# Kernel optimization log

Hardware: AMD Instinct MI355X
Metric: run time of the kernel (lower is better)

Reference implementation:

```python
import math
import jax, jax.numpy as jnp
import numpy as np

B, C_IN, C_OUT, H, W = 8, 256, 256, 64, 64
STYLE_DIM, KSIZE = 512, 3
UP, DOWN = 2, 2          # AliasFreeActivation: upsample = layer_upsample*2 = 2, downsample = 2
N_TAPS = 12
MARGIN = 10


def _kaiser_lowpass(n_taps, cutoff, band_half, sr):
    # lowpass_filter() from the source (1D kaiser-windowed sinc)
    df = 2.0 * band_half / (sr / 2.0)
    atten = 2.285 * (n_taps - 1) * np.pi * df + 7.95
    if atten > 50:
        beta = 0.1102 * (atten - 8.7)
    elif atten >= 21:
        beta = 0.5842 * (atten - 21) ** 0.4 + 0.07886 * (atten - 21)
    else:
        beta = 0.0
    ind = np.arange(n_taps) - (n_taps - 1) / 2.0
    win = np.i0(beta * np.sqrt(1.0 - (2.0 * ind / (n_taps - 1)) ** 2)) / np.i0(beta)
    return (2.0 * cutoff / sr * np.sinc(2.0 * cutoff / sr * ind) * win).astype(np.float32)


def setup_inputs() -> dict:
    key = jax.random.key(0)
    ks = jax.random.split(key, 4)
    return {
        "input": jax.random.normal(ks[0], (B, C_IN, H, W), jnp.float32),
        "style": jax.random.normal(ks[1], (B, STYLE_DIM), jnp.float32),
        "conv_weight": jax.random.normal(ks[2], (C_OUT, C_IN, KSIZE, KSIZE), jnp.float32),
        "mod_w": jax.random.normal(ks[3], (C_IN, STYLE_DIM), jnp.float32),
        "mod_b": jnp.ones((C_IN,), jnp.float32),          # EqualLinear bias_init=1
        "bias": jnp.zeros((C_OUT,), jnp.float32),         # AliasFreeActivation bias
        "up_filter": jnp.asarray(_kaiser_lowpass(N_TAPS, 32.0, 32.0, 128.0)),
        "down_filter": jnp.asarray(_kaiser_lowpass(N_TAPS, 32.0, 32.0, 128.0)),
    }


def _upfirdn1d(x, kern, up, down, pad0, pad1, axis):
    # Separable upfirdn2d: zero-stuff by `up`, pad, TRUE convolution (flipped
    # kernel correlation), then stride-`down`. lax lhs_dilation gives (n-1)*up+1
    # samples vs torch's n*up, so fold the (up-1) trailing zeros into pad1.
    C, k = x.shape[1], kern.shape[0]
    kflip = kern[::-1]
    if axis == 3:  # width
        w = jnp.tile(kflip.reshape(1, 1, 1, k), (C, 1, 1, 1))
        strides, pad, dil = (1, down), ((0, 0), (pad0, pad1 + up - 1)), (1, up)
    else:  # height
        w = jnp.tile(kflip.reshape(1, 1, k, 1), (C, 1, 1, 1))
        strides, pad, dil = (down, 1), ((pad0, pad1 + up - 1), (0, 0)), (up, 1)
    return jax.lax.conv_general_dilated(
        x, w, strides, pad, lhs_dilation=dil, feature_group_count=C,
        dimension_numbers=('NCHW', 'OIHW', 'NCHW'))


def reference(input, style, conv_weight, mod_w, mod_b, bias, up_filter, down_filter):
    # --- ModulatedConv2d (padding=False, demodulate=True, eval: ema_var=1) ---
    scale = 1.0 / math.sqrt(C_IN * KSIZE * KSIZE)
    s = style @ (mod_w.T / math.sqrt(STYLE_DIM)) + mod_b            # (B, C_in)
    w = scale * conv_weight[None] * s[:, None, :, None, None]      # (B, C_out, C_in, k, k)
    demod = jax.lax.rsqrt(jnp.sum(w * w, axis=(2, 3, 4)) + 1e-8)
    w = w * demod[:, :, None, None, None]
    w = w / (1.0 + 1e-8)  # weight / (sqrt(ema_var) + eps), ema_var buffer = 1.0
    out = jax.vmap(lambda xi, wi: jax.lax.conv_general_dilated(
        xi[None], wi, (1, 1), 'VALID',
        dimension_numbers=('NCHW', 'OIHW', 'NCHW'))[0])(input, w)   # (B, C_out, 62, 62)

    # --- AliasFreeActivation ---
    out = out + bias.reshape(1, -1, 1, 1)
    p = N_TAPS - UP
    up0, up1 = (p + 1) // 2 + UP * 2 - 1, p // 2 + UP   # padding=False branch (k==3)
    uf = up_filter * UP                                  # 1D filter gain (applied per axis)
    out = _upfirdn1d(out, uf, UP, 1, up0, up1, axis=3)
    out = _upfirdn1d(out, uf, UP, 1, up0, up1, axis=2)   # (B, C_out, 128, 128)
    out = jnp.where(out >= 0, out, 0.2 * out) * math.sqrt(2.0)  # fused_leaky_relu
    p = N_TAPS - DOWN
    d0, d1 = (p + 1) // 2, p // 2
    out = _upfirdn1d(out, down_filter, 1, DOWN, d0, d1, axis=3)
    out = _upfirdn1d(out, down_filter, 1, DOWN, d0, d1, axis=2)  # (B, C_out, 64, 64)
    # margin crop: m = (MARGIN*UP - MARGIN*DOWN)//2 = 0 -> no crop
    return out
```

## Files before the change

kernel.cpp:

```cpp
#include <hip/hip_runtime.h>
#include <math.h>

#define B_   8
#define CIN  256
#define COUT 256
#define H_   64
#define W_   64
#define HO   62
#define WO   62
#define SDIM 512

#define CSTRIDE 64

typedef __attribute__((ext_vector_type(8))) short bf16x8;
typedef __attribute__((ext_vector_type(4))) float f32x4;

__device__ __forceinline__ unsigned short f2bf(float f) {
    unsigned int u = __float_as_uint(f);
    u += 0x7fffu + ((u >> 16) & 1u);
    return (unsigned short)(u >> 16);
}
__device__ __forceinline__ float bf2f(unsigned short h) {
    return __uint_as_float(((unsigned int)h) << 16);
}


__global__ void mod_kernel(const float* __restrict__ style, const float* __restrict__ mod_w,
                           const float* __restrict__ mod_b, float* __restrict__ s_out,
                           float* __restrict__ zpage) {
    if (blockIdx.x == 0) {
        zpage[threadIdx.x] = 0.f;
        zpage[threadIdx.x + 256] = 0.f;
    }
    int wid = blockIdx.x * 4 + (threadIdx.x >> 6);
    int lane = threadIdx.x & 63;
    int b = wid >> 8, ci = wid & 255;
    float acc = 0.f;
    const float* st = style + b * SDIM;
    const float* mw = mod_w + ci * SDIM;
    for (int i = 0; i < SDIM; i += 64) acc += st[i + lane] * mw[i + lane];
    for (int m = 32; m >= 1; m >>= 1) acc += __shfl_xor(acc, m, 64);
    if (lane == 0) s_out[wid] = acc * 0.04419417382415922f + mod_b[ci];
}

__global__ void wsplit_kernel(const float* __restrict__ cw, float* __restrict__ wsq,
                              unsigned short* __restrict__ wh) {
    int idx = blockIdx.x * blockDim.x + threadIdx.x;
    int co = idx >> 8, ci = idx & 255;
    const float* p = cw + (size_t)idx * 9;
    float ss = 0.f;
#pragma unroll
    for (int k = 0; k < 9; ++k) {
        float v = p[k];
        ss += v * v;
        wh[(k * COUT + co) * CIN + ci] = f2bf(v);
    }
    wsq[idx] = ss;
}

__global__ void demod_kernel(const float* __restrict__ s_in, const float* __restrict__ wsq,
                             float* __restrict__ dm) {
    int wid = blockIdx.x * 4 + (threadIdx.x >> 6);
    int lane = threadIdx.x & 63;
    int b = wid >> 8, co = wid & 255;
    float acc = 0.f;
    for (int i = 0; i < CIN; i += 64) {
        float sv = s_in[b * CIN + i + lane];
        acc += sv * sv * wsq[co * CIN + i + lane];
    }
    for (int m = 32; m >= 1; m >>= 1) acc += __shfl_xor(acc, m, 64);
    if (lane == 0) {
        const float scale = 0.020833333333333332f;
        float demod = rsqrtf(scale * scale * acc + 1e-8f);
        dm[wid] = demod * scale / (1.f + 1e-8f);
    }
}

__global__ __launch_bounds__(256) void xsplit_kernel(
        const float* __restrict__ x, const float* __restrict__ s_in,
        unsigned short* __restrict__ xh) {
    __shared__ float tile[128 * 65];
    __shared__ float s_loc[256];
    int b = blockIdx.x >> 6;
    int y = blockIdx.x & 63;
    int tid = threadIdx.x;
    s_loc[tid] = s_in[(b << 8) + tid];
    __syncthreads();
    for (int half = 0; half < 2; ++half) {
        int cb = half << 7;
        for (int f = tid; f < 2048; f += 256) {
            int ci = f >> 4, x4 = (f & 15) << 2;
            float4 v = *(const float4*)(x + ((((size_t)b << 8) + cb + ci) << 12) + (y << 6) + x4);
            float sv = s_loc[cb + ci];
            float* t = tile + ci * 65 + x4;
            t[0] = v.x * sv; t[1] = v.y * sv; t[2] = v.z * sv; t[3] = v.w * sv;
        }
        __syncthreads();
        for (int g = tid; g < 1024; g += 256) {
            int c = g & 15, xx = g >> 4;
            unsigned int hw[4];
#pragma unroll
            for (int q = 0; q < 4; ++q) {
                float v0 = tile[(c * 8 + 2 * q) * 65 + xx];
                float v1 = tile[(c * 8 + 2 * q + 1) * 65 + xx];
                hw[q] = (unsigned int)f2bf(v0) | ((unsigned int)f2bf(v1) << 16);
            }
            int o = ((((b << 6) + y) << 6) + xx) * 256 + cb + (c << 3);
            *(uint4*)(xh + o) = make_uint4(hw[0], hw[1], hw[2], hw[3]);
        }
        __syncthreads();
    }
}

__device__ __forceinline__ void stage_b(const unsigned short* wh, const int* bsrc,
                                        short* dst, int tid, int kyci) {
#pragma unroll
    for (int j = 0; j < 6; ++j)
        __builtin_amdgcn_global_load_lds(
            (const __attribute__((address_space(1))) unsigned int*)(wh + bsrc[j] + kyci),
            (__attribute__((address_space(3))) unsigned int*)(dst + ((tid + (j << 8)) << 3)),
            16, 0, 0);
}
__device__ __forceinline__ void stage_a(const unsigned short* a0, const unsigned short* a1,
                                        const unsigned short* a2, short* dst, int tid, int ci0) {
    __builtin_amdgcn_global_load_lds(
        (const __attribute__((address_space(1))) unsigned int*)(a0 + ci0),
        (__attribute__((address_space(3))) unsigned int*)(dst + (tid << 3)), 16, 0, 0);
    __builtin_amdgcn_global_load_lds(
        (const __attribute__((address_space(1))) unsigned int*)(a1 + ci0),
        (__attribute__((address_space(3))) unsigned int*)(dst + ((tid + 256) << 3)), 16, 0, 0);
    __builtin_amdgcn_global_load_lds(
        (const __attribute__((address_space(1))) unsigned int*)(a2 + ci0),
        (__attribute__((address_space(3))) unsigned int*)(dst + ((tid + 512) << 3)), 16, 0, 0);
}

template<int KY>
__device__ __forceinline__ void conv_compute(const short* Ah, const short* Bb,
        f32x4 (&acc)[4][4], int lrow, int lch, int wy, int wc) {
#pragma unroll
    for (int kx = 0; kx < 3; ++kx) {
        int colL = lrow + kx;
        int asw = (lch ^ ((colL >> 1) & 3)) << 3;
        bf16x8 ahf[4];
#pragma unroll
        for (int yr = 0; yr < 4; ++yr) {
            int rr = wy * 4 + yr + KY;
            ahf[yr] = *(const bf16x8*)(Ah + (rr * 18 + colL) * 32 + asw);
        }
#pragma unroll
        for (int nt = 0; nt < 4; ++nt) {
            int col = wc * 64 + nt * 16 + lrow;
            int boff = (kx << 12) + (col << 5) + ((lch ^ ((col >> 1) & 3)) << 3);
            bf16x8 bhf = *(const bf16x8*)(Bb + boff);
#pragma unroll
            for (int yr = 0; yr < 4; ++yr)
                acc[yr][nt] = __builtin_amdgcn_mfma_f32_16x16x32_bf16(ahf[yr], bhf, acc[yr][nt], 0, 0, 0);
        }
    }
}

__global__ __launch_bounds__(256) void conv_mfma(
        const unsigned short* __restrict__ xh,
        const unsigned short* __restrict__ wh,
        const unsigned short* __restrict__ zpage,
        const float* __restrict__ dm,
        const float* __restrict__ bias, unsigned short* __restrict__ convout) {
    extern __shared__ short lds[];

    int tid = threadIdx.x;
    int b = blockIdx.z;
    int co0 = blockIdx.y << 7;
    int sx = blockIdx.x & 3, sy = blockIdx.x >> 2;
    int x0 = sx << 4, y0 = sy << 3;
    int wid = tid >> 6, lane = tid & 63;
    int wy = wid >> 1, wc = wid & 1;
    int lrow = lane & 15, lch = lane >> 4;

    int bsrc[6];
#pragma unroll
    for (int j = 0; j < 6; ++j) {
        int u = tid + (j << 8);
        int chunk = u & 3;
        int co = (u >> 2) & 127;
        int kx = u >> 9;
        int cs = chunk ^ ((co >> 1) & 3);
        bsrc[j] = (kx << 16) + ((co0 + co) << 8) + (cs << 3);
    }
    const unsigned short* ap0;
    const unsigned short* ap1;
    const unsigned short* ap2;
#pragma unroll
    for (int k = 0; k < 3; ++k) {
        int u = tid + (k << 8);
        int t2 = u >> 2;
        int col = t2 % 18, row = t2 / 18;
        int yy = y0 + row, xx = x0 + col;
        bool ok = (u < 720) && (yy < 64) && (xx < 64);
        int cs = (u & 3) ^ ((col >> 1) & 3);
        const unsigned short* p = ok ? xh + ((((b << 6) + yy) << 6) + xx) * 256 + (cs << 3) : zpage;
        if (k == 0) ap0 = p; else if (k == 1) ap1 = p; else ap2 = p;
    }

    f32x4 acc[4][4];
#pragma unroll
    for (int i = 0; i < 4; ++i)
#pragma unroll
        for (int j = 0; j < 4; ++j) acc[i][j] = (f32x4){0.f, 0.f, 0.f, 0.f};

    stage_a(ap0, ap1, ap2, lds, tid, 0);
    stage_b(wh, bsrc, lds + 12288, tid, 0);
    __syncthreads();

#pragma unroll 1
    for (int ks = 0; ks < 8; ++ks) {
        int ci0 = ks << 5;
        int ci0n = (ks + 1) << 5;
        int pb = ks & 1;
        short* Acur = lds + (pb ? 6144 : 0);
        short* Anxt = lds + (pb ? 0 : 6144);
        short* Bcur = lds + (pb ? 24576 : 12288);
        short* Balt = lds + (pb ? 12288 : 24576);
        stage_b(wh, bsrc, Balt, tid, 196608 + ci0);
        conv_compute<0>(Acur, Bcur, acc, lrow, lch, wy, wc);
        __syncthreads();
        stage_b(wh, bsrc, Bcur, tid, 2 * 196608 + ci0);
        conv_compute<1>(Acur, Balt, acc, lrow, lch, wy, wc);
        __syncthreads();
        stage_b(wh, bsrc, Balt, tid, ci0n);
        stage_a(ap0, ap1, ap2, Anxt, tid, ci0n);
        conv_compute<2>(Acur, Bcur, acc, lrow, lch, wy, wc);
        __syncthreads();
    }

    int xs4 = x0 + (lch << 2);
#pragma unroll
    for (int nt = 0; nt < 4; ++nt) {
        int co = co0 + wc * 64 + nt * 16 + lrow;
        float dmv = dm[(b << 8) + co];
        float bv = bias[co];
#pragma unroll
        for (int yr = 0; yr < 4; ++yr) {
            int y = y0 + wy * 4 + yr;
            if (y < HO) {
                ushort4 o;
                o.x = f2bf(acc[yr][nt][0] * dmv + bv);
                o.y = f2bf(acc[yr][nt][1] * dmv + bv);
                o.z = f2bf(acc[yr][nt][2] * dmv + bv);
                o.w = f2bf(acc[yr][nt][3] * dmv + bv);
                if (xs4 == 60) { o.z = 0; o.w = 0; }
                *(ushort4*)(convout + ((size_t)((b << 8) + co) * HO + y) * CSTRIDE + xs4) = o;
            }
        }
    }
}

__global__ __launch_bounds__(256) void filter_kernel(
        const unsigned short* __restrict__ convout, const float* __restrict__ upf,
        const float* __restrict__ dnf, float* __restrict__ out) {
    __shared__ __align__(16) float lds0[11672];
    __shared__ __align__(16) float trow2[4][2][144];
    __shared__ float uf[12], df[12];
    float* bufA = lds0 + 2432;
    float* bufB = lds0;
    int tid = threadIdx.x;
    int p = blockIdx.x;
    const unsigned short* src = convout + (size_t)p * (HO * CSTRIDE);
    float* dst = out + (size_t)p * (64 * 64);
    if (tid < 12) { uf[tid] = upf[tid] * 2.f; df[tid] = dnf[tid]; }
    for (int idx = tid; idx < 1056; idx += 256) {
        int r = idx / 132, cc = idx - r * 132;
        bufA[(r < 4 ? r : 62 + r) * 132 + cc] = 0.f;
    }
    for (int idx = tid; idx < 325; idx += 256) bufB[idx] = 0.f;
    __syncthreads();
    for (int task = tid; task < 62 * 16; task += 256) {
        int y = task >> 4, g = task & 15;
        const unsigned short* row = src + y * CSTRIDE + (g << 2);
        ushort4 c0 = (g > 0)  ? *(const ushort4*)(row - 4) : make_ushort4(0, 0, 0, 0);
        ushort4 c1 = *(const ushort4*)(row);
        ushort4 c2 = (g < 15) ? *(const ushort4*)(row + 4) : make_ushort4(0, 0, 0, 0);
        float xv[10];
        xv[0] = bf2f(c0.x); xv[1] = bf2f(c0.y); xv[2] = bf2f(c0.z); xv[3] = bf2f(c0.w);
        xv[4] = bf2f(c1.x); xv[5] = bf2f(c1.y); xv[6] = bf2f(c1.z); xv[7] = bf2f(c1.w);
        xv[8] = bf2f(c2.x); xv[9] = bf2f(c2.y);
        float* arow = bufA + (y + 4) * 132 + (g << 3);
#pragma unroll
        for (int dd = 0; dd < 4; ++dd) {
            float oe = 0.f, oo = 0.f;
#pragma unroll
            for (int v = 0; v < 6; ++v) {
                oe += uf[2 * v + 1] * xv[dd + 5 - v];
                oo += uf[2 * v] * xv[dd + 6 - v];
            }
            *(float2*)(arow + 2 * dd) = make_float2(oe, oo);
        }
    }
    __syncthreads();

    int wid = tid >> 6, lane = tid & 63;
    float* tr0 = &trow2[wid][0][0];
    float* tr1 = &trow2[wid][1][0];
    if (lane < 5) { tr0[lane] = 0.f; tr1[lane] = 0.f; }
    if (lane < 7) { tr0[133 + lane] = 0.f; tr1[133 + lane] = 0.f; }
    const float SQ2 = 1.4142135623730951f;
    float w0[7], w1[7];
#pragma unroll
    for (int d = 0; d < 7; ++d) {
        w0[d] = bufA[(wid + d) * 132 + lane];
        w1[d] = bufA[(wid + d) * 132 + lane + 64];
    }
    for (int it = 0; it < 16; ++it) {
        int n = 4 * it + wid;
        {
            float te0 = 0.f, to0 = 0.f, te1 = 0.f, to1 = 0.f;
#pragma unroll
            for (int d = 0; d < 6; ++d) { te0 += uf[11 - 2 * d] * w0[d]; te1 += uf[11 - 2 * d] * w1[d]; }
#pragma unroll
            for (int d = 1; d < 7; ++d) { to0 += uf[12 - 2 * d] * w0[d]; to1 += uf[12 - 2 * d] * w1[d]; }
            te0 = (te0 >= 0.f ? te0 : 0.2f * te0) * SQ2;
            to0 = (to0 >= 0.f ? to0 : 0.2f * to0) * SQ2;
            te1 = (te1 >= 0.f ? te1 : 0.2f * te1) * SQ2;
            to1 = (to1 >= 0.f ? to1 : 0.2f * to1) * SQ2;
            tr0[5 + lane] = te0;      tr1[5 + lane] = to0;
            tr0[69 + lane] = te1;     tr1[69 + lane] = to1;
        }
        __builtin_amdgcn_wave_barrier();
        {
            int xo = lane;
            const float2* a0 = (const float2*)&tr0[2 * xo];
            const float2* a1 = (const float2*)&tr1[2 * xo];
            float v0[12], v1[12];
#pragma unroll
            for (int q = 0; q < 6; ++q) {
                float2 u0 = a0[q], u1 = a1[q];
                v0[2 * q] = u0.x; v0[2 * q + 1] = u0.y;
                v1[2 * q] = u1.x; v1[2 * q + 1] = u1.y;
            }
            float s0 = 0.f, s1 = 0.f;
#pragma unroll
            for (int u = 0; u < 12; ++u) {
                s0 += df[u] * v0[11 - u];
                s1 += df[u] * v1[11 - u];
            }
            bufB[(2 * n + 5) * 65 + xo] = s0;
            bufB[(2 * n + 6) * 65 + xo] = s1;
        }
        if (it < 15) {
#pragma unroll
            for (int d = 0; d < 3; ++d) { w0[d] = w0[d + 4]; w1[d] = w1[d + 4]; }
#pragma unroll
            for (int d = 3; d < 7; ++d) {
                w0[d] = bufA[(n + 4 + d) * 132 + lane];
                w1[d] = bufA[(n + 4 + d) * 132 + lane + 64];
            }
        }
        if ((it & 3) == 3) __syncthreads();
        else __builtin_amdgcn_wave_barrier();
    }
    for (int idx = tid; idx < 64 * 64; idx += 256) {
        int yo = idx >> 6, xx = idx & 63;
        float acc2 = 0.f;
#pragma unroll
        for (int u = 0; u < 12; ++u) {
            int rr = 2 * yo + 6 - u;
            float v = (rr < 128) ? bufB[(rr + 5) * 65 + xx] : 0.f;
            acc2 += df[u] * v;
        }
        dst[idx] = acc2;
    }
}

extern "C" void kernel_launch(void* const* d_in, const int* in_sizes, int n_in,
                              void* d_out, int out_size, void* d_ws, size_t ws_size,
                              hipStream_t stream) {
    const float* input       = (const float*)d_in[0];
    const float* style       = (const float*)d_in[1];
    const float* conv_weight = (const float*)d_in[2];
    const float* mod_w       = (const float*)d_in[3];
    const float* mod_b       = (const float*)d_in[4];
    const float* bias        = (const float*)d_in[5];
    const float* up_filter   = (const float*)d_in[6];
    const float* down_filter = (const float*)d_in[7];
    float* ws  = (float*)d_ws;
    float* out = (float*)d_out;
    float* s_buf   = ws;
    float* dm      = ws + 2048;
    float* wsq     = ws + 4096;
    unsigned short* wh      = (unsigned short*)(ws + 69632);
    float* zpage            = ws + 364544;
    unsigned short* xh      = (unsigned short*)(ws + 659456);
    unsigned short* convout = (unsigned short*)(ws + 9048064);

    hipLaunchKernelGGL(mod_kernel, dim3(512), dim3(256), 0, stream, style, mod_w, mod_b, s_buf, zpage);
    hipLaunchKernelGGL(wsplit_kernel, dim3(256), dim3(256), 0, stream, conv_weight, wsq, wh);
    hipLaunchKernelGGL(demod_kernel, dim3(512), dim3(256), 0, stream, s_buf, wsq, dm);
    hipLaunchKernelGGL(xsplit_kernel, dim3(512), dim3(256), 0, stream, input, s_buf, xh);
    hipLaunchKernelGGL(conv_mfma, dim3(32, 2, 8), dim3(256), 73728, stream,
                       xh, wh, (const unsigned short*)zpage, dm, bias, convout);
    hipLaunchKernelGGL(filter_kernel, dim3(2048), dim3(256), 0, stream,
                       convout, up_filter, down_filter, out);
}
```

Before: 118.2 us.

## Reorder filter stage: vertical up+lrelu+down in registers, then horizontal downsample

The filter kernel now does the vertical upsample, leaky ReLU and vertical downsample per column in a register ring buffer of 13 rows. Each thread owns one of 128 upsampled columns and handles half the rows, with a small overlap between the two halves. The horizontal downsample then runs from an intermediate LDS tile. This removes the per-row wave barriers, the block-wide syncs and the transpose-style LDS round trips. In exchange it uses more LDS (about 73KB), which may lower occupancy, recomputes the overlapping rows, and relies on heavy unrolling with higher register pressure.

```diff
diff --git a/kernel.cpp b/kernel.cpp
--- a/kernel.cpp
+++ b/kernel.cpp
@@ -254,14 +254,66 @@
     }
 }
 
+template<int N0, int NSTEPS, int KSTART>
+__device__ __forceinline__ void vpipe(const float* __restrict__ bufA,
+                                      float* __restrict__ C, int c,
+                                      const float* __restrict__ uf,
+                                      const float* __restrict__ df) {
+    const float SQ2 = 1.4142135623730951f;
+    float ufr[12], dfr[12];
+#pragma unroll
+    for (int i = 0; i < 12; ++i) { ufr[i] = uf[i]; dfr[i] = df[i]; }
+    float w[7];
+#pragma unroll
+    for (int d = 0; d < 7; ++d) w[d] = bufA[(N0 + d) * 132 + c];
+    float pcur = bufA[((N0 + 7) > 69 ? 69 : (N0 + 7)) * 132 + c];
+    float t[13];
+#pragma unroll
+    for (int i = 0; i < 13; ++i) t[i] = 0.f;
+#pragma unroll
+    for (int k = 0; k < NSTEPS; ++k) {
+        const int n = N0 + k;
+        const int rnext = (n + 8) > 69 ? 69 : (n + 8);
+        float pnext = bufA[rnext * 132 + c];
+        float te = 0.f, to = 0.f;
+#pragma unroll
+        for (int d = 0; d < 6; ++d) te += ufr[11 - 2 * d] * w[d];
+#pragma unroll
+        for (int d = 1; d < 7; ++d) to += ufr[12 - 2 * d] * w[d];
+        te = (te >= 0.f ? te : 0.2f * te) * SQ2;
+        to = (to >= 0.f ? to : 0.2f * to) * SQ2;
+        if (2 * n < 128) {
+            t[(2 * n) % 13] = te;
+            t[(2 * n + 1) % 13] = to;
+        } else {
+            t[(2 * n) % 13] = 0.f;
+            t[(2 * n + 1) % 13] = 0.f;
+        }
+        if (k >= KSTART) {
+            const int yo = n - 3;
+            float acc = 0.f;
+#pragma unroll
+            for (int u = 0; u < 12; ++u) {
+                const int r = 2 * n - u;
+                const int ri = ((r % 13) + 13) % 13;
+                acc += dfr[u] * t[ri];
+            }
+            C[yo * 140 + 5 + c] = acc;
+        }
+#pragma unroll
+        for (int d = 0; d < 6; ++d) w[d] = w[d + 1];
+        w[6] = pcur;
+        pcur = pnext;
+    }
+}
+
 __global__ __launch_bounds__(256) void filter_kernel(
         const unsigned short* __restrict__ convout, const float* __restrict__ upf,
         const float* __restrict__ dnf, float* __restrict__ out) {
-    __shared__ __align__(16) float lds0[11672];
-    __shared__ __align__(16) float trow2[4][2][144];
+    __shared__ __align__(16) float lds0[18200];
     __shared__ float uf[12], df[12];
-    float* bufA = lds0 + 2432;
-    float* bufB = lds0;
+    float* bufA = lds0;
+    float* C    = lds0 + 9240;
     int tid = threadIdx.x;
     int p = blockIdx.x;
     const unsigned short* src = convout + (size_t)p * (HO * CSTRIDE);
@@ -271,7 +323,10 @@
         int r = idx / 132, cc = idx - r * 132;
         bufA[(r < 4 ? r : 62 + r) * 132 + cc] = 0.f;
     }
-    for (int idx = tid; idx < 325; idx += 256) bufB[idx] = 0.f;
+    for (int idx = tid; idx < 640; idx += 256) {
+        int r = idx / 10, q = idx - r * 10;
+        C[r * 140 + (q < 5 ? q : 128 + q)] = 0.f;
+    }
     __syncthreads();
     for (int task = tid; task < 62 * 16; task += 256) {
         int y = task >> 4, g = task & 15;
@@ -296,76 +351,25 @@
         }
     }
     __syncthreads();
-
-    int wid = tid >> 6, lane = tid & 63;
-    float* tr0 = &trow2[wid][0][0];
-    float* tr1 = &trow2[wid][1][0];
-    if (lane < 5) { tr0[lane] = 0.f; tr1[lane] = 0.f; }
-    if (lane < 7) { tr0[133 + lane] = 0.f; tr1[133 + lane] = 0.f; }
-    const float SQ2 = 1.4142135623730951f;
-    float w0[7], w1[7];
-#pragma unroll
-    for (int d = 0; d < 7; ++d) {
-        w0[d] = bufA[(wid + d) * 132 + lane];
-        w1[d] = bufA[(wid + d) * 132 + lane + 64];
-    }
-    for (int it = 0; it < 16; ++it) {
-        int n = 4 * it + wid;
-        {
-            float te0 = 0.f, to0 = 0.f, te1 = 0.f, to1 = 0.f;
-#pragma unroll
-            for (int d = 0; d < 6; ++d) { te0 += uf[11 - 2 * d] * w0[d]; te1 += uf[11 - 2 * d] * w1[d]; }
-#pragma unroll
-            for (int d = 1; d < 7; ++d) { to0 += uf[12 - 2 * d] * w0[d]; to1 += uf[12 - 2 * d] * w1[d]; }
-            te0 = (te0 >= 0.f ? te0 : 0.2f * te0) * SQ2;
-            to0 = (to0 >= 0.f ? to0 : 0.2f * to0) * SQ2;
-            te1 = (te1 >= 0.f ? te1 : 0.2f * te1) * SQ2;
-            to1 = (to1 >= 0.f ? to1 : 0.2f * to1) * SQ2;
-            tr0[5 + lane] = te0;      tr1[5 + lane] = to0;
-            tr0[69 + lane] = te1;     tr1[69 + lane] = to1;
-        }
-        __builtin_amdgcn_wave_barrier();
-        {
-            int xo = lane;
-            const float2* a0 = (const float2*)&tr0[2 * xo];
-            const float2* a1 = (const float2*)&tr1[2 * xo];
-            float v0[12], v1[12];
-#pragma unroll
-            for (int q = 0; q < 6; ++q) {
-                float2 u0 = a0[q], u1 = a1[q];
-                v0[2 * q] = u0.x; v0[2 * q + 1] = u0.y;
-                v1[2 * q] = u1.x; v1[2 * q + 1] = u1.y;
-            }
-            float s0 = 0.f, s1 = 0.f;
-#pragma unroll
-            for (int u = 0; u < 12; ++u) {
-                s0 += df[u] * v0[11 - u];
-                s1 += df[u] * v1[11 - u];
-            }
-            bufB[(2 * n + 5) * 65 + xo] = s0;
-            bufB[(2 * n + 6) * 65 + xo] = s1;
-        }
-        if (it < 15) {
-#pragma unroll
-            for (int d = 0; d < 3; ++d) { w0[d] = w0[d + 4]; w1[d] = w1[d + 4]; }
-#pragma unroll
-            for (int d = 3; d < 7; ++d) {
-                w0[d] = bufA[(n + 4 + d) * 132 + lane];
-                w1[d] = bufA[(n + 4 + d) * 132 + lane + 64];
-            }
-        }
-        if ((it & 3) == 3) __syncthreads();
-        else __builtin_amdgcn_wave_barrier();
-    }
+    {
+        const int c = tid & 127;
+        const int h = tid >> 7;
+        if (h == 0) vpipe<0, 35, 3>(bufA, C, c, uf, df);
+        else        vpipe<29, 38, 6>(bufA, C, c, uf, df);
+    }
+    __syncthreads();
     for (int idx = tid; idx < 64 * 64; idx += 256) {
-        int yo = idx >> 6, xx = idx & 63;
+        int yo = idx >> 6, xo = idx & 63;
+        const float2* a = (const float2*)&C[yo * 140 + 2 * xo];
+        float v[12];
+#pragma unroll
+        for (int q = 0; q < 6; ++q) {
+            float2 u2 = a[q];
+            v[2 * q] = u2.x; v[2 * q + 1] = u2.y;
+        }
         float acc2 = 0.f;
 #pragma unroll
-        for (int u = 0; u < 12; ++u) {
-            int rr = 2 * yo + 6 - u;
-            float v = (rr < 128) ? bufB[(rr + 5) * 65 + xx] : 0.f;
-            acc2 += df[u] * v;
-        }
+        for (int u = 0; u < 12; ++u) acc2 += df[u] * v[11 - u];
         dst[idx] = acc2;
     }
 }
```

Result: faster. 104.8 us (-11.3%).
